# Optimization experiments

Measured on AMD Instinct MI355X. Metric: run time of the kernel, lower is better.

## Reference

```python
import jax, jax.numpy as jnp
import numpy as np

# TaskAttention config (from MultiTask_Agg defaults)
B, T, M, C, H, K = 4, 3, 4096, 768, 12, 256  # batch, num_tasks, feature tokens, dim, heads, capacity_factor
HD = C // H
SCALE = HD ** -0.5


def setup_inputs() -> dict:
    key = jax.random.key(0)
    ks = jax.random.split(key, 5)
    x = jax.random.normal(ks[0], (B, T + M, C), jnp.float32)
    # per-task q projections (torch Linear: y = x @ W.T + b)
    Wq = jax.random.normal(ks[1], (T, C, C), jnp.float32) * 0.02
    bq = jnp.zeros((T, C), jnp.float32)
    # shared kv projection
    Wkv = jax.random.normal(ks[2], (2 * C, C), jnp.float32) * 0.02
    bkv = jnp.zeros((2 * C,), jnp.float32)
    # per-task experts (bias=False)
    Wexp = jax.random.normal(ks[3], (T, C, C), jnp.float32) * 0.02
    return {"x": x, "Wq": Wq, "bq": bq, "Wkv": Wkv, "bkv": bkv, "Wexp": Wexp}


def reference(x, Wq, bq, Wkv, bkv, Wexp):
    Bs = x.shape[0]
    feat = x[:, T:, :]                                             # (B,M,C)
    fm = feat.reshape(Bs, M, H, HD).transpose(0, 2, 1, 3)          # (B,H,M,hd)
    kv = feat @ Wkv.T + bkv                                        # (B,M,2C)
    kv = kv.reshape(Bs, M, 2, H, HD).transpose(2, 0, 3, 1, 4)      # (2,B,H,M,hd)
    k, v = kv[0], kv[1]
    tasks = x[:, :T, :]                                            # (B,T,C)
    q = jnp.einsum('btc,tdc->btd', tasks, Wq) + bq                 # per-task Linear
    q = q.reshape(Bs, T, H, HD).transpose(0, 2, 1, 3)              # (B,H,T,hd)
    attn = jnp.einsum('bhtd,bhmd->bhtm', q, k) * SCALE             # (B,H,T,M)
    vals, idx = jax.lax.top_k(attn, K)                             # (B,H,T,K)
    w = jax.nn.softmax(vals, axis=-1)                              # softmax over top-k only
    # attn_token: sparse combine of v at top-k indices (scatter->matmul == gather->weighted sum, indices unique)
    v_topk = jnp.take_along_axis(v[:, :, None, :, :], idx[..., None], axis=3)   # (B,H,T,K,hd)
    attn_token = jnp.einsum('bhtk,bhtkd->bhtd', w, v_topk)
    attn_token = attn_token.transpose(0, 2, 1, 3).reshape(Bs, T, C)             # (B,T,C)
    # gather raw multihead features at top-k, weight, scatter back into dense (B,H,T,M,hd)
    f_topk = jnp.take_along_axis(fm[:, :, None, :, :], idx[..., None], axis=3) * w[..., None]
    bi = jnp.arange(Bs)[:, None, None, None]
    hi = jnp.arange(H)[None, :, None, None]
    ti = jnp.arange(T)[None, None, :, None]
    feature_pad = jnp.zeros((Bs, H, T, M, HD), x.dtype).at[bi, hi, ti, idx].set(f_topk)
    feature_pad = feature_pad.transpose(0, 2, 3, 1, 4).reshape(Bs, T, M, C)     # (B,T,M,C)
    # per-task expert linears (bias=False)
    feature_output = jnp.einsum('btmc,tdc->btmd', feature_pad, Wexp)            # (B,T,M,C)
    token_output = jnp.einsum('btc,tdc->btd', attn_token, Wexp)                 # (B,T,C)
    # task_topk_weight is all-ones => einsum 'btnc,btnc->bnc' is a sum over tasks
    feature_sum = feature_output.sum(axis=1)                                    # (B,M,C)
    return jnp.concatenate([token_output, feature_sum], axis=1)                 # (B,T+M,C)
```

## Files before the change

kernel.cpp:

```cpp
#include <hip/hip_runtime.h>
#include <hip/hip_bf16.h>

#define B_ 4
#define T_ 3
#define M_ 4096
#define C_ 768
#define H_ 12
#define K_ 256
#define HD_ 64
#define TM_ 4099
#define SCALE_ 0.125f
#define NBLK_ 144

typedef __attribute__((ext_vector_type(8))) short bf16x8;
typedef __attribute__((ext_vector_type(4))) float f32x4;

__device__ __forceinline__ unsigned keyf(float f) {
  unsigned u = __float_as_uint(f);
  return (u & 0x80000000u) ? ~u : (u | 0x80000000u);
}

__device__ __forceinline__ unsigned short f2bf(float f) {
  unsigned u = __float_as_uint(f);
  unsigned r = (u + 0x7FFFu + ((u >> 16) & 1u)) >> 16;
  return (unsigned short)r;
}
__device__ __forceinline__ float bf2f(unsigned short u) {
  return __uint_as_float(((unsigned)u) << 16);
}
__device__ __forceinline__ unsigned pk2(float a, float b) {
  return (unsigned)f2bf(a) | ((unsigned)f2bf(b) << 16);
}

__device__ __forceinline__ int block_excl_scan256(int v, int tid, int* sbuf) {
  int lane = tid & 63, wid = tid >> 6;
  int x = v;
  #pragma unroll
  for (int off = 1; off < 64; off <<= 1) {
    int y = __shfl_up(x, off, 64);
    if (lane >= off) x += y;
  }
  if (lane == 63) sbuf[wid] = x;
  __syncthreads();
  int base = 0;
  #pragma unroll
  for (int w = 0; w < 3; ++w) base += (w < wid) ? sbuf[w] : 0;
  __syncthreads();
  return base + x - v;
}


__global__ __launch_bounds__(256) void q_kernel(const float* __restrict__ x,
                                                const float* __restrict__ Wq,
                                                const float* __restrict__ bq,
                                                float* __restrict__ qbuf) {
  int t = blockIdx.x;
  int d0 = blockIdx.y * 64;
  int tid = threadIdx.x;
  __shared__ float ar[B_][C_];
  for (int i = tid; i < B_ * C_; i += 256) {
    int bb = i / C_, c = i % C_;
    ar[bb][c] = x[((size_t)(bb * TM_ + t)) * C_ + c];
  }
  __syncthreads();
  int grp = tid >> 4, ln = tid & 15;
  #pragma unroll
  for (int j = 0; j < 4; ++j) {
    int d = d0 + grp * 4 + j;
    const float4* wr = (const float4*)(Wq + ((size_t)t * C_ + d) * C_);
    float a0 = 0.f, a1 = 0.f, a2 = 0.f, a3 = 0.f;
    #pragma unroll
    for (int it = 0; it < 12; ++it) {
      float4 w4 = wr[ln + 16 * it];
      const float4 x0 = *(const float4*)&ar[0][(ln + 16 * it) * 4];
      const float4 x1 = *(const float4*)&ar[1][(ln + 16 * it) * 4];
      const float4 x2 = *(const float4*)&ar[2][(ln + 16 * it) * 4];
      const float4 x3 = *(const float4*)&ar[3][(ln + 16 * it) * 4];
      a0 += w4.x * x0.x + w4.y * x0.y + w4.z * x0.z + w4.w * x0.w;
      a1 += w4.x * x1.x + w4.y * x1.y + w4.z * x1.z + w4.w * x1.w;
      a2 += w4.x * x2.x + w4.y * x2.y + w4.z * x2.z + w4.w * x2.w;
      a3 += w4.x * x3.x + w4.y * x3.y + w4.z * x3.z + w4.w * x3.w;
    }
    #pragma unroll
    for (int off = 1; off < 16; off <<= 1) {
      a0 += __shfl_xor(a0, off, 16);
      a1 += __shfl_xor(a1, off, 16);
      a2 += __shfl_xor(a2, off, 16);
      a3 += __shfl_xor(a3, off, 16);
    }
    if (ln == 0) {
      float bqv = bq[t * C_ + d];
      qbuf[(size_t)(0 * T_ + t) * C_ + d] = a0 + bqv;
      qbuf[(size_t)(1 * T_ + t) * C_ + d] = a1 + bqv;
      qbuf[(size_t)(2 * T_ + t) * C_ + d] = a2 + bqv;
      qbuf[(size_t)(3 * T_ + t) * C_ + d] = a3 + bqv;
    }
  }
}

__global__ __launch_bounds__(256) void sprj_kernel(const float* __restrict__ qbuf,
                                                   const float* __restrict__ Wkv,
                                                   const float* __restrict__ bkv,
                                                   float* __restrict__ sprjT,
                                                   float* __restrict__ qbb,
                                                   uint4* __restrict__ bucketz) {
  int blk = blockIdx.x;
  int j = blk % 36;
  int b = blk / 36;
  int t = j % T_;
  int h = j / T_;
  int tid = threadIdx.x;
  {
    uint4 z = make_uint4(0u, 0u, 0u, 0u);
    int base = blk * 256 + tid;
    #pragma unroll
    for (int i = 0; i < 4; ++i) bucketz[i * 36864 + base] = z;
  }
  __shared__ float qs[HD_];
  if (tid < HD_) qs[tid] = qbuf[((size_t)(b * T_ + t)) * C_ + h * HD_ + tid];
  __syncthreads();
  if (tid == 0) {
    float s = 0.f;
    for (int i = 0; i < HD_; ++i) s += qs[i] * bkv[h * HD_ + i];
    qbb[blk] = s;
  }
  float a0 = 0.f, a1 = 0.f, a2 = 0.f;
  for (int i = 0; i < HD_; ++i) {
    const float* wr = Wkv + ((size_t)(h * HD_ + i)) * C_;
    float qi = qs[i];
    a0 += qi * wr[tid];
    a1 += qi * wr[tid + 256];
    a2 += qi * wr[tid + 512];
  }
  sprjT[((size_t)b * C_ + tid) * 36 + j] = a0;
  sprjT[((size_t)b * C_ + tid + 256) * 36 + j] = a1;
  sprjT[((size_t)b * C_ + tid + 512) * 36 + j] = a2;
}

__global__ __launch_bounds__(256) void score_kernel(const float* __restrict__ x,
                                                    const float* __restrict__ sprjT,
                                                    float* __restrict__ scp) {
  int b = blockIdx.x;
  int m0 = blockIdx.y * 256;
  int cc = blockIdx.z;
  int tid = threadIdx.x;

  __shared__ float fl[32][256];

  float acc[36];
  #pragma unroll
  for (int j = 0; j < 36; ++j) acc[j] = 0.f;

  const float* fr0 = x + ((size_t)(b * TM_ + T_ + m0 + tid)) * C_ + cc * 64;

  for (int kc = 0; kc < 2; ++kc) {
    float4 v[8];
    const float4* fr = (const float4*)(fr0 + kc * 32);
    #pragma unroll
    for (int i = 0; i < 8; ++i) v[i] = fr[i];
    __syncthreads();
    #pragma unroll
    for (int i = 0; i < 8; ++i) {
      fl[i * 4 + 0][tid] = v[i].x;
      fl[i * 4 + 1][tid] = v[i].y;
      fl[i * 4 + 2][tid] = v[i].z;
      fl[i * 4 + 3][tid] = v[i].w;
    }
    __syncthreads();
    const float* sp = sprjT + ((size_t)b * C_ + cc * 64 + kc * 32) * 36;
    #pragma unroll 4
    for (int k = 0; k < 32; ++k) {
      float f = fl[k][tid];
      const float* sr = sp + k * 36;
      #pragma unroll
      for (int j = 0; j < 36; ++j) acc[j] += f * sr[j];
    }
  }
  float* op = scp + ((size_t)cc * NBLK_ + (size_t)b * 36) * M_ + m0 + tid;
  #pragma unroll
  for (int j = 0; j < 36; ++j) op[(size_t)j * M_] = acc[j];
}

__global__ __launch_bounds__(256) void score_reduce(const float* __restrict__ scp,
                                                    const float* __restrict__ qbb,
                                                    float* __restrict__ scg) {
  int blk = blockIdx.x;
  int m = blockIdx.y * 1024 + threadIdx.x * 4;
  float qb = qbb[blk];
  float4 s = make_float4(qb, qb, qb, qb);
  #pragma unroll
  for (int cc = 0; cc < 12; ++cc) {
    float4 a = *(const float4*)&scp[((size_t)cc * NBLK_ + blk) * M_ + m];
    s.x += a.x; s.y += a.y; s.z += a.z; s.w += a.w;
  }
  float4 o;
  o.x = s.x * SCALE_;
  o.y = s.y * SCALE_;
  o.z = s.z * SCALE_;
  o.w = s.w * SCALE_;
  *(float4*)&scg[(size_t)blk * M_ + m] = o;
}

__global__ __launch_bounds__(256) void topk_kernel(const float* __restrict__ scg,
                                                   int* __restrict__ ibuf,
                                                   float* __restrict__ wbuf,
                                                   int* __restrict__ bucket) {
  int blk = blockIdx.x;
  int tid = threadIdx.x;

  __shared__ float sc[M_];
  __shared__ unsigned hist[256];
  __shared__ int sbuf[4];
  __shared__ int selm[K_];
  __shared__ float redf[4];
  __shared__ int sh_bin, sh_rem;

  const float4* srow = (const float4*)(scg + (size_t)blk * M_);
  for (int i = tid; i < M_ / 4; i += 256) ((float4*)sc)[i] = srow[i];
  __syncthreads();

  unsigned prefix = 0;
  int remaining = K_;
  for (int shift = 24; shift >= 0; shift -= 8) {
    hist[tid] = 0;
    __syncthreads();
    unsigned pmask = (shift == 24) ? 0u : (0xFFFFFFFFu << (shift + 8));
    #pragma unroll 4
    for (int i = 0; i < 16; ++i) {
      unsigned k = keyf(sc[tid * 16 + i]);
      if ((k & pmask) == prefix) atomicAdd(&hist[(k >> shift) & 255u], 1u);
    }
    __syncthreads();
    int bin = 255 - tid;
    int v = (int)hist[bin];
    int cex = block_excl_scan256(v, tid, sbuf);
    if (cex < remaining && cex + v >= remaining) {
      sh_bin = bin;
      sh_rem = remaining - cex;
    }
    __syncthreads();
    prefix |= ((unsigned)sh_bin) << shift;
    remaining = sh_rem;
    __syncthreads();
  }
  const unsigned tau = prefix;
  const int r = remaining;
  const int cgt = K_ - r;

  int base = tid * 16;
  int myCnt = 0, myTie = 0;
  #pragma unroll
  for (int i = 0; i < 16; i++) {
    unsigned k = keyf(sc[base + i]);
    myCnt += (k > tau);
    myTie += (k == tau);
  }
  int offs = block_excl_scan256(myCnt, tid, sbuf);
  int toffs = block_excl_scan256(myTie, tid, sbuf);
  for (int i = 0; i < 16; i++) {
    int m = base + i;
    unsigned k = keyf(sc[m]);
    if (k > tau) {
      selm[offs++] = m;
    } else if (k == tau) {
      if (toffs < r) selm[cgt + toffs] = m;
      toffs++;
    }
  }
  __syncthreads();

  int m = selm[tid];
  float val = sc[m];
  float mx = val;
  #pragma unroll
  for (int off = 32; off > 0; off >>= 1) mx = fmaxf(mx, __shfl_xor(mx, off, 64));
  if ((tid & 63) == 0) redf[tid >> 6] = mx;
  __syncthreads();
  mx = fmaxf(fmaxf(redf[0], redf[1]), fmaxf(redf[2], redf[3]));
  float e = expf(val - mx);
  float sm = e;
  #pragma unroll
  for (int off = 32; off > 0; off >>= 1) sm += __shfl_xor(sm, off, 64);
  __syncthreads();
  if ((tid & 63) == 0) redf[tid >> 6] = sm;
  __syncthreads();
  sm = redf[0] + redf[1] + redf[2] + redf[3];
  ibuf[(size_t)blk * K_ + tid] = m;
  wbuf[(size_t)blk * K_ + tid] = e / sm;
  bucket[((size_t)(blk / 36) * M_ + m) * 36 + (blk % 36)] = tid + 1;
}

__global__ __launch_bounds__(256) void wfeat_kernel(const float* __restrict__ x,
                                                    const int* __restrict__ ibuf,
                                                    const float* __restrict__ wbuf,
                                                    float* __restrict__ wfp) {
  int blk = blockIdx.x, kc = blockIdx.y, cseg = blockIdx.z;
  int b = blk / 36;
  int tid = threadIdx.x;
  __shared__ int ml[64];
  __shared__ float wl[64];
  if (tid < 64) {
    ml[tid] = ibuf[(size_t)blk * K_ + kc * 64 + tid];
    wl[tid] = wbuf[(size_t)blk * K_ + kc * 64 + tid];
  }
  __syncthreads();
  int c = cseg * 256 + tid;
  const float* fbase = x + ((size_t)b * TM_ + T_) * C_ + c;
  float a = 0.f;
  #pragma unroll 4
  for (int kk = 0; kk < 64; ++kk) {
    a += wl[kk] * fbase[(size_t)ml[kk] * C_];
  }
  wfp[((size_t)blk * 4 + kc) * C_ + c] = a;
}

__global__ __launch_bounds__(256) void attn_token_kernel(
    const float* __restrict__ wfp, const float* __restrict__ Wkv,
    const float* __restrict__ bkv, float* __restrict__ atbuf) {
  int blk = blockIdx.x;
  int t = blk % T_;
  int h = (blk / T_) % H_;
  int b = blk / (T_ * H_);
  int tid = threadIdx.x;
  __shared__ float wfeat[C_];
  const float* p0 = wfp + ((size_t)blk * 4) * C_;
  #pragma unroll
  for (int j = 0; j < 3; ++j) {
    int c = tid + j * 256;
    wfeat[c] = p0[c] + p0[C_ + c] + p0[2 * C_ + c] + p0[3 * C_ + c];
  }
  __syncthreads();
  int grp = tid >> 4, ln = tid & 15;
  for (int rr = grp; rr < HD_; rr += 16) {
    const float4* wr = (const float4*)(Wkv + ((size_t)(C_ + h * HD_ + rr)) * C_);
    float acc = 0.f;
    #pragma unroll
    for (int it = 0; it < 12; ++it) {
      float4 wv = wr[ln + it * 16];
      const float4 fv = *(const float4*)&wfeat[(ln + it * 16) * 4];
      acc += wv.x * fv.x + wv.y * fv.y + wv.z * fv.z + wv.w * fv.w;
    }
    acc += __shfl_xor(acc, 1, 16);
    acc += __shfl_xor(acc, 2, 16);
    acc += __shfl_xor(acc, 4, 16);
    acc += __shfl_xor(acc, 8, 16);
    if (ln == 0)
      atbuf[((size_t)(b * T_ + t)) * C_ + h * HD_ + rr] =
          acc + bkv[C_ + h * HD_ + rr];
  }
}

__global__ __launch_bounds__(256) void token_out(const float* __restrict__ atbuf,
                                                 const float* __restrict__ Wexp,
                                                 float* __restrict__ out) {
  int t = blockIdx.x;
  int d0 = blockIdx.y * 64;
  int tid = threadIdx.x;
  __shared__ float ar[B_][C_];
  for (int i = tid; i < B_ * C_; i += 256) {
    int bb = i / C_, c = i % C_;
    ar[bb][c] = atbuf[((size_t)(bb * T_ + t)) * C_ + c];
  }
  __syncthreads();
  int grp = tid >> 4, ln = tid & 15;
  #pragma unroll
  for (int j = 0; j < 4; ++j) {
    int d = d0 + grp * 4 + j;
    const float4* wr = (const float4*)(Wexp + ((size_t)t * C_ + d) * C_);
    float a0 = 0.f, a1 = 0.f, a2 = 0.f, a3 = 0.f;
    #pragma unroll
    for (int it = 0; it < 12; ++it) {
      float4 w4 = wr[ln + 16 * it];
      const float4 x0 = *(const float4*)&ar[0][(ln + 16 * it) * 4];
      const float4 x1 = *(const float4*)&ar[1][(ln + 16 * it) * 4];
      const float4 x2 = *(const float4*)&ar[2][(ln + 16 * it) * 4];
      const float4 x3 = *(const float4*)&ar[3][(ln + 16 * it) * 4];
      a0 += w4.x * x0.x + w4.y * x0.y + w4.z * x0.z + w4.w * x0.w;
      a1 += w4.x * x1.x + w4.y * x1.y + w4.z * x1.z + w4.w * x1.w;
      a2 += w4.x * x2.x + w4.y * x2.y + w4.z * x2.z + w4.w * x2.w;
      a3 += w4.x * x3.x + w4.y * x3.y + w4.z * x3.z + w4.w * x3.w;
    }
    #pragma unroll
    for (int off = 1; off < 16; off <<= 1) {
      a0 += __shfl_xor(a0, off, 16);
      a1 += __shfl_xor(a1, off, 16);
      a2 += __shfl_xor(a2, off, 16);
      a3 += __shfl_xor(a3, off, 16);
    }
    if (ln == 0) {
      out[((size_t)0 * TM_ + t) * C_ + d] = a0;
      out[((size_t)1 * TM_ + t) * C_ + d] = a1;
      out[((size_t)2 * TM_ + t) * C_ + d] = a2;
      out[((size_t)3 * TM_ + t) * C_ + d] = a3;
    }
  }
}

__global__ __launch_bounds__(256) void scatter_mfma(
    const float* __restrict__ x, const float* __restrict__ Wexp,
    const int* __restrict__ ibuf, const float* __restrict__ wbuf,
    unsigned short* __restrict__ Y) {
  int th = blockIdx.x;
  int h = th / T_, t = th % T_;
  int b = blockIdx.y >> 2, ks = blockIdx.y & 3;
  int bht = b * 36 + th;
  int tid = threadIdx.x;

  __shared__ unsigned short fw[64][72];
  __shared__ unsigned short wt[192][72];

  {
    int kk = tid >> 2, cp = (tid & 3) * 16;
    int sel = ks * 64 + kk;
    int m = ibuf[(size_t)bht * K_ + sel];
    float w = wbuf[(size_t)bht * K_ + sel];
    const float* fr = x + ((size_t)(b * TM_) + T_ + m) * C_ + h * HD_ + cp;
    float4 f0 = *(const float4*)(fr + 0);
    float4 f1 = *(const float4*)(fr + 4);
    float4 f2 = *(const float4*)(fr + 8);
    float4 f3 = *(const float4*)(fr + 12);
    uint4 u0 = make_uint4(pk2(f0.x * w, f0.y * w), pk2(f0.z * w, f0.w * w),
                          pk2(f1.x * w, f1.y * w), pk2(f1.z * w, f1.w * w));
    uint4 u1 = make_uint4(pk2(f2.x * w, f2.y * w), pk2(f2.z * w, f2.w * w),
                          pk2(f3.x * w, f3.y * w), pk2(f3.z * w, f3.w * w));
    *(uint4*)&fw[kk][cp] = u0;
    *(uint4*)&fw[kk][cp + 8] = u1;
  }
  __syncthreads();

  int lane = tid & 63, wave = tid >> 6;
  int lrow = lane & 15, lk8 = (lane >> 4) * 8, g4 = (lane >> 4) * 4;

  for (int dc = 0; dc < 4; ++dc) {
    {
      #pragma unroll
      for (int r2 = 0; r2 < 3; ++r2) {
        int idx = r2 * 256 + tid;
        int dd = idx >> 2, cq = (idx & 3) * 16;
        const float* wr =
            Wexp + ((size_t)t * C_ + dc * 192 + dd) * C_ + h * HD_ + cq;
        float4 f0 = *(const float4*)(wr + 0);
        float4 f1 = *(const float4*)(wr + 4);
        float4 f2 = *(const float4*)(wr + 8);
        float4 f3 = *(const float4*)(wr + 12);
        uint4 u0 = make_uint4(pk2(f0.x, f0.y), pk2(f0.z, f0.w),
                              pk2(f1.x, f1.y), pk2(f1.z, f1.w));
        uint4 u1 = make_uint4(pk2(f2.x, f2.y), pk2(f2.z, f2.w),
                              pk2(f3.x, f3.y), pk2(f3.z, f3.w));
        *(uint4*)&wt[dd][cq] = u0;
        *(uint4*)&wt[dd][cq + 8] = u1;
      }
    }
    __syncthreads();

    f32x4 acc[12];
    #pragma unroll
    for (int n = 0; n < 12; ++n) acc[n] = (f32x4){0.f, 0.f, 0.f, 0.f};

    #pragma unroll
    for (int ks2 = 0; ks2 < 2; ++ks2) {
      bf16x8 a = *(const bf16x8*)&fw[wave * 16 + lrow][ks2 * 32 + lk8];
      #pragma unroll
      for (int n = 0; n < 12; ++n) {
        bf16x8 bfr = *(const bf16x8*)&wt[n * 16 + lrow][ks2 * 32 + lk8];
        acc[n] = __builtin_amdgcn_mfma_f32_16x16x32_bf16(a, bfr, acc[n], 0, 0, 0);
      }
    }

    #pragma unroll
    for (int n = 0; n < 12; ++n) {
      int d = dc * 192 + n * 16 + lrow;
      #pragma unroll
      for (int q = 0; q < 4; ++q) {
        int row = ks * 64 + wave * 16 + g4 + q;
        Y[((size_t)bht * K_ + row) * C_ + d] = f2bf(acc[n][q]);
      }
    }
    __syncthreads();
  }
}

__global__ __launch_bounds__(256) void combine_kernel(
    const unsigned short* __restrict__ Y, const int* __restrict__ bucket,
    float* __restrict__ out) {
  int wave = threadIdx.x >> 6, lane = threadIdx.x & 63;
  int bm = blockIdx.x * 4 + wave;
  int b = bm / M_, m = bm % M_;
  const int* bk = bucket + (size_t)bm * 36;
  int v = (lane < 36) ? bk[lane] : 0;
  unsigned long long mask = __ballot(v > 0);
  float a[12] = {0.f};
  while (mask) {
    int th = __ffsll((unsigned long long)mask) - 1;
    mask &= mask - 1;
    int sel = __shfl(v, th) - 1;
    const unsigned short* yr = Y + ((size_t)(b * 36 + th) * K_ + sel) * C_;
    #pragma unroll
    for (int seg = 0; seg < 3; ++seg) {
      uint2 r = *(const uint2*)(yr + seg * 256 + lane * 4);
      a[seg * 4 + 0] += bf2f((unsigned short)(r.x & 0xFFFFu));
      a[seg * 4 + 1] += bf2f((unsigned short)(r.x >> 16));
      a[seg * 4 + 2] += bf2f((unsigned short)(r.y & 0xFFFFu));
      a[seg * 4 + 3] += bf2f((unsigned short)(r.y >> 16));
    }
  }
  float* orow = out + ((size_t)b * TM_ + T_ + m) * C_;
  #pragma unroll
  for (int seg = 0; seg < 3; ++seg) {
    float4 o = make_float4(a[seg * 4 + 0], a[seg * 4 + 1], a[seg * 4 + 2],
                           a[seg * 4 + 3]);
    *(float4*)(orow + seg * 256 + lane * 4) = o;
  }
}

extern "C" void kernel_launch(void* const* d_in, const int* in_sizes, int n_in,
                              void* d_out, int out_size, void* d_ws, size_t ws_size,
                              hipStream_t stream) {
  (void)in_sizes; (void)n_in; (void)ws_size; (void)out_size;
  const float* x = (const float*)d_in[0];
  const float* Wq = (const float*)d_in[1];
  const float* bq = (const float*)d_in[2];
  const float* Wkv = (const float*)d_in[3];
  const float* bkv = (const float*)d_in[4];
  const float* Wexp = (const float*)d_in[5];
  float* out = (float*)d_out;

  char* ws = (char*)d_ws;
  float* qbuf = (float*)ws;
  float* atbuf = (float*)(ws + 36864);
  int* ibuf = (int*)(ws + 73728);
  float* wbuf = (float*)(ws + 221184);
  float* sprjT = (float*)(ws + 368640);
  float* qbb = (float*)(ws + 811008);
  float* wfp = (float*)(ws + 812032);
  int* bucket = (int*)(ws + 2581504);
  float* scg = (float*)(ws + 4940800);
  float* scp = (float*)(ws + 7300096);
  unsigned short* Ybf = (unsigned short*)(ws + 7300096);

  q_kernel<<<dim3(T_, 12), 256, 0, stream>>>(x, Wq, bq, qbuf);
  sprj_kernel<<<NBLK_, 256, 0, stream>>>(qbuf, Wkv, bkv, sprjT, qbb,
                                         (uint4*)bucket);
  score_kernel<<<dim3(B_, 16, 12), 256, 0, stream>>>(x, sprjT, scp);
  score_reduce<<<dim3(NBLK_, 4), 256, 0, stream>>>(scp, qbb, scg);
  topk_kernel<<<NBLK_, 256, 0, stream>>>(scg, ibuf, wbuf, bucket);
  wfeat_kernel<<<dim3(NBLK_, 4, 3), 256, 0, stream>>>(x, ibuf, wbuf, wfp);
  attn_token_kernel<<<NBLK_, 256, 0, stream>>>(wfp, Wkv, bkv, atbuf);
  token_out<<<dim3(T_, 12), 256, 0, stream>>>(atbuf, Wexp, out);
  scatter_mfma<<<dim3(36, 16), 256, 0, stream>>>(x, Wexp, ibuf, wbuf, Ybf);
  combine_kernel<<<B_ * M_ / 4, 256, 0, stream>>>(Ybf, bucket, out);
}
```

Baseline: 139.0 us.

## Shrink bucket to u16, swap MFMA operands for packed Y stores, reorder grid

Measured after the change: 149.9 us. 1.08x slower.

```diff
diff --git a/kernel.cpp b/kernel.cpp
--- a/kernel.cpp
+++ b/kernel.cpp
@@ -113,8 +113,8 @@
   {
     uint4 z = make_uint4(0u, 0u, 0u, 0u);
     int base = blk * 256 + tid;
-    #pragma unroll
-    for (int i = 0; i < 4; ++i) bucketz[i * 36864 + base] = z;
+    bucketz[base] = z;
+    bucketz[36864 + base] = z;
   }
   __shared__ float qs[HD_];
   if (tid < HD_) qs[tid] = qbuf[((size_t)(b * T_ + t)) * C_ + h * HD_ + tid];
@@ -204,7 +204,7 @@
 __global__ __launch_bounds__(256) void topk_kernel(const float* __restrict__ scg,
                                                    int* __restrict__ ibuf,
                                                    float* __restrict__ wbuf,
-                                                   int* __restrict__ bucket) {
+                                                   unsigned short* __restrict__ bucket) {
   int blk = blockIdx.x;
   int tid = threadIdx.x;
 
@@ -287,7 +287,8 @@
   sm = redf[0] + redf[1] + redf[2] + redf[3];
   ibuf[(size_t)blk * K_ + tid] = m;
   wbuf[(size_t)blk * K_ + tid] = e / sm;
-  bucket[((size_t)(blk / 36) * M_ + m) * 36 + (blk % 36)] = tid + 1;
+  bucket[((size_t)(blk / 36) * M_ + m) * 36 + (blk % 36)] =
+      (unsigned short)(tid + 1);
 }
 
 __global__ __launch_bounds__(256) void wfeat_kernel(const float* __restrict__ x,
@@ -400,9 +401,9 @@
     const float* __restrict__ x, const float* __restrict__ Wexp,
     const int* __restrict__ ibuf, const float* __restrict__ wbuf,
     unsigned short* __restrict__ Y) {
-  int th = blockIdx.x;
+  int th = blockIdx.y;
   int h = th / T_, t = th % T_;
-  int b = blockIdx.y >> 2, ks = blockIdx.y & 3;
+  int b = blockIdx.x >> 2, ks = blockIdx.x & 3;
   int bht = b * 36 + th;
   int tid = threadIdx.x;
 
@@ -430,6 +431,9 @@
 
   int lane = tid & 63, wave = tid >> 6;
   int lrow = lane & 15, lk8 = (lane >> 4) * 8, g4 = (lane >> 4) * 4;
+
+  int sel = ks * 64 + wave * 16 + lrow;
+  unsigned short* yrow = Y + ((size_t)bht * K_ + sel) * C_;
 
   for (int dc = 0; dc < 4; ++dc) {
     {
@@ -459,35 +463,34 @@
 
     #pragma unroll
     for (int ks2 = 0; ks2 < 2; ++ks2) {
-      bf16x8 a = *(const bf16x8*)&fw[wave * 16 + lrow][ks2 * 32 + lk8];
+      bf16x8 bfw = *(const bf16x8*)&fw[wave * 16 + lrow][ks2 * 32 + lk8];
       #pragma unroll
       for (int n = 0; n < 12; ++n) {
-        bf16x8 bfr = *(const bf16x8*)&wt[n * 16 + lrow][ks2 * 32 + lk8];
-        acc[n] = __builtin_amdgcn_mfma_f32_16x16x32_bf16(a, bfr, acc[n], 0, 0, 0);
+        bf16x8 awt = *(const bf16x8*)&wt[n * 16 + lrow][ks2 * 32 + lk8];
+        acc[n] = __builtin_amdgcn_mfma_f32_16x16x32_bf16(awt, bfw, acc[n], 0, 0, 0);
       }
     }
 
     #pragma unroll
     for (int n = 0; n < 12; ++n) {
-      int d = dc * 192 + n * 16 + lrow;
-      #pragma unroll
-      for (int q = 0; q < 4; ++q) {
-        int row = ks * 64 + wave * 16 + g4 + q;
-        Y[((size_t)bht * K_ + row) * C_ + d] = f2bf(acc[n][q]);
-      }
+      int dbase = dc * 192 + n * 16 + g4;
+      uint2 p;
+      p.x = pk2(acc[n][0], acc[n][1]);
+      p.y = pk2(acc[n][2], acc[n][3]);
+      *(uint2*)(yrow + dbase) = p;
     }
     __syncthreads();
   }
 }
 
 __global__ __launch_bounds__(256) void combine_kernel(
-    const unsigned short* __restrict__ Y, const int* __restrict__ bucket,
+    const unsigned short* __restrict__ Y, const unsigned short* __restrict__ bucket,
     float* __restrict__ out) {
   int wave = threadIdx.x >> 6, lane = threadIdx.x & 63;
   int bm = blockIdx.x * 4 + wave;
   int b = bm / M_, m = bm % M_;
-  const int* bk = bucket + (size_t)bm * 36;
-  int v = (lane < 36) ? bk[lane] : 0;
+  const unsigned short* bk = bucket + (size_t)bm * 36;
+  int v = (lane < 36) ? (int)bk[lane] : 0;
   unsigned long long mask = __ballot(v > 0);
   float a[12] = {0.f};
   while (mask) {
@@ -533,10 +536,10 @@
   float* sprjT = (float*)(ws + 368640);
   float* qbb = (float*)(ws + 811008);
   float* wfp = (float*)(ws + 812032);
-  int* bucket = (int*)(ws + 2581504);
-  float* scg = (float*)(ws + 4940800);
-  float* scp = (float*)(ws + 7300096);
-  unsigned short* Ybf = (unsigned short*)(ws + 7300096);
+  unsigned short* bucket = (unsigned short*)(ws + 2581504);
+  float* scg = (float*)(ws + 3761152);
+  float* scp = (float*)(ws + 6120448);
+  unsigned short* Ybf = (unsigned short*)(ws + 6120448);
 
   q_kernel<<<dim3(T_, 12), 256, 0, stream>>>(x, Wq, bq, qbuf);
   sprj_kernel<<<NBLK_, 256, 0, stream>>>(qbuf, Wkv, bkv, sprjT, qbb,
@@ -547,6 +550,6 @@
   wfeat_kernel<<<dim3(NBLK_, 4, 3), 256, 0, stream>>>(x, ibuf, wbuf, wfp);
   attn_token_kernel<<<NBLK_, 256, 0, stream>>>(wfp, Wkv, bkv, atbuf);
   token_out<<<dim3(T_, 12), 256, 0, stream>>>(atbuf, Wexp, out);
-  scatter_mfma<<<dim3(36, 16), 256, 0, stream>>>(x, Wexp, ibuf, wbuf, Ybf);
+  scatter_mfma<<<dim3(16, 36), 256, 0, stream>>>(x, Wexp, ibuf, wbuf, Ybf);
   combine_kernel<<<B_ * M_ / 4, 256, 0, stream>>>(Ybf, bucket, out);
 }
```
